# Kernel tuning notes

Hardware: AMD Instinct MI355X
Metric: run time of the kernel (lower is better)

The kernel has to match this reference:

```python
import jax, jax.numpy as jnp
import numpy as np

NEG_SLOPE = 0.2


def gat_conv(x, src, dst, W, att_src, att_dst, bias, heads, out_ch):
    # x: [N, Fin]; src/dst: [E] (self-loops already included)
    N = x.shape[0]
    h = (x @ W).reshape(N, heads, out_ch)                      # [N, H, C]
    a_s = jnp.einsum('nhc,hc->nh', h, att_src)                 # [N, H]
    a_d = jnp.einsum('nhc,hc->nh', h, att_dst)                 # [N, H]
    e = jax.nn.leaky_relu(a_s[src] + a_d[dst], NEG_SLOPE)      # [E, H]
    # segment softmax over incoming edges of each dst node
    e_max = jax.ops.segment_max(e, dst, num_segments=N)        # [N, H]
    p = jnp.exp(e - e_max[dst])                                # [E, H]
    denom = jax.ops.segment_sum(p, dst, num_segments=N)        # [N, H]
    alpha = p / denom[dst]                                     # [E, H]
    msg = h[src] * alpha[:, :, None]                           # [E, H, C]
    out = jax.ops.segment_sum(msg, dst, num_segments=N)        # [N, H, C]
    return out.reshape(N, heads * out_ch) + bias


def setup_inputs() -> dict:
    key = jax.random.key(0)
    ks = jax.random.split(key, 10)
    N, E, F_IN, HID, HEADS, NCLS = 100000, 3200000, 512, 8, 8, 16
    x = jax.random.normal(ks[0], (N, F_IN), dtype=jnp.float32)
    edge_index = jax.random.randint(ks[1], (2, E), 0, N, dtype=jnp.int64)
    s = 1.0 / np.sqrt(F_IN)
    W1 = jax.random.uniform(ks[2], (F_IN, HEADS * HID), jnp.float32, -s, s)
    att_src1 = jax.random.normal(ks[3], (HEADS, HID), jnp.float32) * 0.1
    att_dst1 = jax.random.normal(ks[4], (HEADS, HID), jnp.float32) * 0.1
    b1 = jnp.zeros((HEADS * HID,), jnp.float32)
    s2 = 1.0 / np.sqrt(HEADS * HID)
    W2 = jax.random.uniform(ks[5], (HEADS * HID, NCLS), jnp.float32, -s2, s2)
    att_src2 = jax.random.normal(ks[6], (1, NCLS), jnp.float32) * 0.1
    att_dst2 = jax.random.normal(ks[7], (1, NCLS), jnp.float32) * 0.1
    b2 = jnp.zeros((NCLS,), jnp.float32)
    return {"x": x, "edge_index": edge_index, "W1": W1, "att_src1": att_src1,
            "att_dst1": att_dst1, "b1": b1, "W2": W2, "att_src2": att_src2,
            "att_dst2": att_dst2, "b2": b2}


def reference(x, edge_index, W1, att_src1, att_dst1, b1, W2, att_src2, att_dst2, b2):
    N = x.shape[0]
    loops = jnp.arange(N, dtype=edge_index.dtype)
    src = jnp.concatenate([edge_index[0], loops])  # PyG add_self_loops=True
    dst = jnp.concatenate([edge_index[1], loops])
    # eval mode: F.dropout is identity
    h = gat_conv(x, src, dst, W1, att_src1, att_dst1, b1, heads=8, out_ch=8)
    h = jax.nn.elu(h)
    out = gat_conv(h, src, dst, W2, att_src2, att_dst2, b2, heads=1, out_ch=16)
    return out
```

## Files before the change

kernel.cpp:

```cpp
#include <hip/hip_runtime.h>

#define F_IN 512
#define F1 64
#define NCLS 16
#define NEG_SLOPE 0.2f

typedef __attribute__((ext_vector_type(8))) short short8;
typedef __attribute__((ext_vector_type(4))) float f32x4;

__device__ __forceinline__ unsigned short f2bf(float f) {
    unsigned u = __float_as_uint(f);
    return (unsigned short)((u + 0x7fffu + ((u >> 16) & 1u)) >> 16);
}
__device__ __forceinline__ float bf2f(unsigned short u) {
    return __uint_as_float(((unsigned)u) << 16);
}


__global__ __launch_bounds__(64) void k_detect(const int* __restrict__ ei, int E,
                                               unsigned* __restrict__ mode) {
    int t = threadIdx.x;
    unsigned nz = 0;
    int lim = (E > 256) ? 256 : E;
    for (int k = t; k < lim; k += 64) nz |= (unsigned)ei[2 * k + 1];
    for (int off = 1; off < 64; off <<= 1) nz |= __shfl_xor(nz, off);
    if (t == 0) *mode = (nz == 0) ? 1u : 0u;
}


__device__ __forceinline__ void gemm1_tile(const float* __restrict__ x,
                                           const float* __restrict__ W1,
                                           const float* __restrict__ att_s,
                                           const float* __restrict__ att_d,
                                           unsigned short* __restrict__ h1b,
                                           float* __restrict__ a_s1,
                                           float* __restrict__ a_d1,
                                           int N, int row0,
                                           unsigned short (*Abuf)[40],
                                           unsigned short (*BbufT)[40]) {
    const int tid = threadIdx.x;
    const int w = tid >> 6, lane = tid & 63;
    const int quad = lane >> 4, r16 = lane & 15;

    f32x4 acc[4];
#pragma unroll
    for (int t = 0; t < 4; t++) acc[t] = (f32x4){0.f, 0.f, 0.f, 0.f};

    const int a_row = tid >> 2;
    const int a_seg = (tid & 3) * 8;
    const int b_col = tid & 63;
    const int b_kq  = tid >> 6;
    const int ar = row0 + a_row;

    for (int k0 = 0; k0 < F_IN; k0 += 32) {
        {
            float4 v0 = make_float4(0.f, 0.f, 0.f, 0.f), v1 = v0;
            if (ar < N) {
                const float* xp = x + (size_t)ar * F_IN + k0 + a_seg;
                v0 = *(const float4*)xp;
                v1 = *(const float4*)(xp + 4);
            }
            short8 cv;
            cv[0] = (short)f2bf(v0.x); cv[1] = (short)f2bf(v0.y);
            cv[2] = (short)f2bf(v0.z); cv[3] = (short)f2bf(v0.w);
            cv[4] = (short)f2bf(v1.x); cv[5] = (short)f2bf(v1.y);
            cv[6] = (short)f2bf(v1.z); cv[7] = (short)f2bf(v1.w);
            *(short8*)&Abuf[a_row][a_seg] = cv;
        }
        {
            const float* wp = W1 + (size_t)(k0 + b_kq * 8) * F1 + b_col;
            short8 cv;
#pragma unroll
            for (int j = 0; j < 8; j++)
                cv[j] = (short)f2bf(wp[(size_t)j * F1]);
            *(short8*)&BbufT[b_col][b_kq * 8] = cv;
        }
        __syncthreads();

        short8 af = *(const short8*)&Abuf[w * 16 + r16][quad * 8];
#pragma unroll
        for (int t = 0; t < 4; t++) {
            short8 bf = *(const short8*)&BbufT[t * 16 + r16][quad * 8];
            acc[t] = __builtin_amdgcn_mfma_f32_16x16x32_bf16(af, bf, acc[t], 0, 0, 0);
        }
        __syncthreads();
    }

    float ats[4], atd[4];
#pragma unroll
    for (int t = 0; t < 4; t++) {
        ats[t] = att_s[t * 16 + r16];
        atd[t] = att_d[t * 16 + r16];
    }
#pragma unroll
    for (int r = 0; r < 4; r++) {
        int grow = row0 + w * 16 + quad * 4 + r;
        bool ok = grow < N;
        float ps[4], pd[4];
#pragma unroll
        for (int t = 0; t < 4; t++) {
            float vv = acc[t][r];
            if (ok) h1b[(size_t)grow * F1 + t * 16 + r16] = f2bf(vv);
            ps[t] = vv * ats[t];
            pd[t] = vv * atd[t];
        }
#pragma unroll
        for (int t = 0; t < 4; t++) {
            ps[t] += __shfl_xor(ps[t], 1); pd[t] += __shfl_xor(pd[t], 1);
            ps[t] += __shfl_xor(ps[t], 2); pd[t] += __shfl_xor(pd[t], 2);
            ps[t] += __shfl_xor(ps[t], 4); pd[t] += __shfl_xor(pd[t], 4);
        }
        if (ok && (r16 & 7) == 0) {
            int hh0 = r16 >> 3;
#pragma unroll
            for (int t = 0; t < 4; t++) {
                a_s1[(size_t)grow * 8 + t * 2 + hh0] = ps[t];
                a_d1[(size_t)grow * 8 + t * 2 + hh0] = pd[t];
            }
        }
    }
}


__global__ __launch_bounds__(256) void k_fusedA(const float* __restrict__ x,
                                                const float* __restrict__ W1,
                                                const float* __restrict__ att_s,
                                                const float* __restrict__ att_d,
                                                unsigned short* __restrict__ h1b,
                                                float* __restrict__ a_s1,
                                                float* __restrict__ a_d1, int N,
                                                const int* __restrict__ ei,
                                                const unsigned* __restrict__ mode,
                                                int* __restrict__ src32,
                                                int* __restrict__ dst32,
                                                unsigned* __restrict__ deg,
                                                unsigned* __restrict__ bucketCnt,
                                                int E, int ET, int nch,
                                                int nb, int shift) {
    __shared__ __align__(16) char smem[10240];
    unsigned b = blockIdx.x;
    if ((b & 1) == 0) {
        gemm1_tile(x, W1, att_s, att_d, h1b, a_s1, a_d1, N, (int)(b >> 1) * 64,
                   (unsigned short (*)[40])smem,
                   (unsigned short (*)[40])(smem + 5120));
        return;
    }
    unsigned* cntL = (unsigned*)smem;
    for (int i = threadIdx.x; i < 1024; i += 256) cntL[i] = 0u;
    __syncthreads();

    const unsigned stride = (unsigned)nch * 256u;
    unsigned t = (b >> 1) * 256u + threadIdx.x;
    bool m64 = (*mode != 0u);
    const long long* e64 = (const long long*)ei;
    unsigned i = t;
    for (; i + 3u * stride < (unsigned)ET; i += 4u * stride) {
        unsigned i0 = i, i1 = i + stride, i2 = i + 2u * stride, i3 = i + 3u * stride;
        int s0, v0, s1, v1, s2, v2, s3, v3;
        if (m64) {
            s0 = (int)e64[i0]; s1 = (int)e64[i1]; s2 = (int)e64[i2]; s3 = (int)e64[i3];
            v0 = (i0 < (unsigned)E) ? (int)e64[E + i0] : (int)(i0 - E);
            v1 = (i1 < (unsigned)E) ? (int)e64[E + i1] : (int)(i1 - E);
            v2 = (i2 < (unsigned)E) ? (int)e64[E + i2] : (int)(i2 - E);
            v3 = (i3 < (unsigned)E) ? (int)e64[E + i3] : (int)(i3 - E);
        } else {
            s0 = ei[i0]; s1 = ei[i1]; s2 = ei[i2]; s3 = ei[i3];
            v0 = (i0 < (unsigned)E) ? ei[E + i0] : (int)(i0 - E);
            v1 = (i1 < (unsigned)E) ? ei[E + i1] : (int)(i1 - E);
            v2 = (i2 < (unsigned)E) ? ei[E + i2] : (int)(i2 - E);
            v3 = (i3 < (unsigned)E) ? ei[E + i3] : (int)(i3 - E);
        }
        if (i0 >= (unsigned)E) s0 = (int)(i0 - E);
        if (i1 >= (unsigned)E) s1 = (int)(i1 - E);
        if (i2 >= (unsigned)E) s2 = (int)(i2 - E);
        if (i3 >= (unsigned)E) s3 = (int)(i3 - E);
        s0 = s0 < 0 ? 0 : (s0 >= N ? N - 1 : s0);  v0 = v0 < 0 ? 0 : (v0 >= N ? N - 1 : v0);
        s1 = s1 < 0 ? 0 : (s1 >= N ? N - 1 : s1);  v1 = v1 < 0 ? 0 : (v1 >= N ? N - 1 : v1);
        s2 = s2 < 0 ? 0 : (s2 >= N ? N - 1 : s2);  v2 = v2 < 0 ? 0 : (v2 >= N ? N - 1 : v2);
        s3 = s3 < 0 ? 0 : (s3 >= N ? N - 1 : s3);  v3 = v3 < 0 ? 0 : (v3 >= N ? N - 1 : v3);
        src32[i0] = s0; dst32[i0] = v0;
        src32[i1] = s1; dst32[i1] = v1;
        src32[i2] = s2; dst32[i2] = v2;
        src32[i3] = s3; dst32[i3] = v3;
        atomicAdd(&deg[v0], 1u);
        atomicAdd(&deg[v1], 1u);
        atomicAdd(&deg[v2], 1u);
        atomicAdd(&deg[v3], 1u);
        atomicAdd(&cntL[(unsigned)v0 >> shift], 1u);
        atomicAdd(&cntL[(unsigned)v1 >> shift], 1u);
        atomicAdd(&cntL[(unsigned)v2 >> shift], 1u);
        atomicAdd(&cntL[(unsigned)v3 >> shift], 1u);
    }
    for (; i < (unsigned)ET; i += stride) {
        int s, v;
        if (i < (unsigned)E) {
            if (m64) { s = (int)e64[i]; v = (int)e64[E + i]; }
            else     { s = ei[i];       v = ei[E + i]; }
        } else {
            s = v = (int)(i - E);
        }
        s = s < 0 ? 0 : (s >= N ? N - 1 : s);
        v = v < 0 ? 0 : (v >= N ? N - 1 : v);
        src32[i] = s; dst32[i] = v;
        atomicAdd(&deg[v], 1u);
        atomicAdd(&cntL[(unsigned)v >> shift], 1u);
    }
    __syncthreads();
    for (int k = threadIdx.x; k < nb; k += 256) {
        unsigned c = cntL[k];
        if (c) atomicAdd(&bucketCnt[k], c);
    }
}


__global__ __launch_bounds__(256) void k_fusedB(const float* __restrict__ x,
                                                const float* __restrict__ W1,
                                                const float* __restrict__ att_s,
                                                const float* __restrict__ att_d,
                                                unsigned short* __restrict__ h1b,
                                                float* __restrict__ a_s1,
                                                float* __restrict__ a_d1, int N,
                                                int rowSplit,
                                                const int* __restrict__ src32,
                                                const int* __restrict__ dst32,
                                                unsigned* __restrict__ bucketFill,
                                                unsigned* __restrict__ pairs,
                                                int ET, int nch,
                                                int nb, int shift) {
    __shared__ __align__(16) char smem[10240];
    unsigned b = blockIdx.x;
    if (b & 1) {
        gemm1_tile(x, W1, att_s, att_d, h1b, a_s1, a_d1, N,
                   rowSplit + (int)(b >> 1) * 64,
                   (unsigned short (*)[40])smem,
                   (unsigned short (*)[40])(smem + 5120));
        return;
    }
    unsigned* cntA = (unsigned*)smem;
    unsigned* ofsA = (unsigned*)(smem + 4096);
    unsigned* part = (unsigned*)(smem + 8192);
    const int t = threadIdx.x;
    const int chunk = (ET + nch - 1) / nch;
    const int cbase = (int)(b >> 1) * chunk;
    const int cend = (cbase + chunk < ET) ? cbase + chunk : ET;
    const unsigned lmask = (1u << shift) - 1u;

    for (int k = t; k < 1024; k += 256) cntA[k] = 0u;
    __syncthreads();
    for (int k = cbase + t; k < cend; k += 256)
        atomicAdd(&cntA[(unsigned)dst32[k] >> shift], 1u);
    __syncthreads();
    unsigned a0 = cntA[4 * t + 0], a1 = cntA[4 * t + 1];
    unsigned a2 = cntA[4 * t + 2], a3 = cntA[4 * t + 3];
    unsigned ssum = a0 + a1 + a2 + a3;
    part[t] = ssum;
    __syncthreads();
    for (int off = 1; off < 256; off <<= 1) {
        unsigned add = (t >= off) ? part[t - off] : 0u;
        __syncthreads();
        part[t] += add;
        __syncthreads();
    }
    unsigned excl = part[t] - ssum;
    ofsA[4 * t + 0] = excl;
    ofsA[4 * t + 1] = excl + a0;
    ofsA[4 * t + 2] = excl + a0 + a1;
    ofsA[4 * t + 3] = excl + a0 + a1 + a2;
    __syncthreads();
    for (int k = t; k < nb; k += 256) {
        unsigned c = cntA[k];
        unsigned g = c ? atomicAdd(&bucketFill[k], c) : 0u;
        cntA[k] = g - ofsA[k];
    }
    __syncthreads();
    for (int k = cbase + t; k < cend; k += 256) {
        int v = dst32[k];
        int s = src32[k];
        unsigned bb = (unsigned)v >> shift;
        unsigned slot = atomicAdd(&ofsA[bb], 1u);
        pairs[cntA[bb] + slot] = (unsigned)s | (((unsigned)v & lmask) << 20);
    }
}


__global__ __launch_bounds__(256) void k_tilesum(const unsigned* __restrict__ deg,
                                                 int N, unsigned* __restrict__ tileSum) {
    int tid = threadIdx.x;
    int v = blockIdx.x * 256 + tid;
    unsigned d = (v < N) ? deg[v] : 0u;
    for (int off = 1; off < 64; off <<= 1) d += __shfl_xor(d, off);
    __shared__ unsigned ps[4];
    int lane = tid & 63, wid = tid >> 6;
    if (lane == 0) ps[wid] = d;
    __syncthreads();
    if (tid == 0) tileSum[blockIdx.x] = ps[0] + ps[1] + ps[2] + ps[3];
}

__global__ __launch_bounds__(1024) void k_scan_tiles(const unsigned* __restrict__ tileSum,
                                                     int nt, unsigned* __restrict__ tileOfs) {
    __shared__ unsigned sbuf[1024];
    int t = threadIdx.x;
    unsigned val = (t < nt) ? tileSum[t] : 0u;
    sbuf[t] = val;
    __syncthreads();
    for (int off = 1; off < 1024; off <<= 1) {
        unsigned add = (t >= off) ? sbuf[t - off] : 0u;
        __syncthreads();
        sbuf[t] += add;
        __syncthreads();
    }
    if (t < nt) tileOfs[t] = sbuf[t] - val;
}

__global__ __launch_bounds__(1024) void k_scan_buckets(const unsigned* __restrict__ bucketCnt,
                                                       int nb,
                                                       unsigned* __restrict__ bucketOfs,
                                                       unsigned* __restrict__ bucketFill) {
    __shared__ unsigned sbuf[1024];
    int t = threadIdx.x;
    unsigned val = (t < nb) ? bucketCnt[t] : 0u;
    sbuf[t] = val;
    __syncthreads();
    for (int off = 1; off < 1024; off <<= 1) {
        unsigned add = (t >= off) ? sbuf[t - off] : 0u;
        __syncthreads();
        sbuf[t] += add;
        __syncthreads();
    }
    if (t < nb) {
        unsigned e = sbuf[t] - val;
        bucketOfs[t] = e;
        bucketFill[t] = e;
    }
}

__global__ __launch_bounds__(256) void k_rowptr(const unsigned* __restrict__ deg,
                                                const unsigned* __restrict__ tileOfs,
                                                unsigned* __restrict__ row_ptr,
                                                int N, int ET) {
    __shared__ unsigned sbuf[256];
    int t = threadIdx.x;
    int v = blockIdx.x * 256 + t;
    unsigned d = (v < N) ? deg[v] : 0u;
    sbuf[t] = d;
    __syncthreads();
    for (int off = 1; off < 256; off <<= 1) {
        unsigned add = (t >= off) ? sbuf[t - off] : 0u;
        __syncthreads();
        sbuf[t] += add;
        __syncthreads();
    }
    if (v < N) row_ptr[v] = tileOfs[blockIdx.x] + sbuf[t] - d;
    if (blockIdx.x == 0 && t == 0) row_ptr[N] = (unsigned)ET;
}


__global__ __launch_bounds__(256) void k_sort(const unsigned* __restrict__ pairs,
                                              const unsigned* __restrict__ bucketOfs,
                                              const unsigned* __restrict__ bucketCnt,
                                              const unsigned* __restrict__ row_ptr,
                                              unsigned* __restrict__ ssrc,
                                              int N, int shift) {
    __shared__ unsigned f[1024];
    __shared__ unsigned rbase[1024];
    const int b = blockIdx.x;
    const int t = threadIdx.x;
    const int nodes = 1 << shift;
    const int bbase = b << shift;
    for (int i = t; i < nodes; i += 256) {
        f[i] = 0u;
        int v = bbase + i;
        rbase[i] = (v < N) ? row_ptr[v] : 0u;
    }
    __syncthreads();
    const unsigned base = bucketOfs[b];
    const unsigned cnt = bucketCnt[b];
    for (unsigned i = (unsigned)t; i < cnt; i += 256u) {
        unsigned pk = pairs[base + i];
        unsigned s = pk & 0xFFFFFu;
        unsigned local = pk >> 20;
        unsigned pos = rbase[local] + atomicAdd(&f[local], 1u);
        ssrc[pos] = s;
    }
}


__global__ __launch_bounds__(256) void k_agg1(const unsigned short* __restrict__ h1b,
                                              const float* __restrict__ a_s1,
                                              const float* __restrict__ a_d1,
                                              const float* __restrict__ b1,
                                              const unsigned* __restrict__ row_ptr,
                                              const unsigned* __restrict__ ssrc,
                                              float* __restrict__ g, int N) {
    int wid = threadIdx.x >> 6, lane = threadIdx.x & 63;
    int v = blockIdx.x * 4 + wid;
    if (v >= N) return;
    unsigned base = row_ptr[v];
    unsigned deg = row_ptr[v + 1] - base;
    int h = lane >> 3;
    float adv = a_d1[(size_t)v * 8 + h];

    float denom = 0.f, acc = 0.f;
    unsigned j = 0;
    for (; j + 8 <= deg; j += 8) {
        unsigned s0 = ssrc[base + j + 0];
        unsigned s1 = ssrc[base + j + 1];
        unsigned s2 = ssrc[base + j + 2];
        unsigned s3 = ssrc[base + j + 3];
        unsigned s4 = ssrc[base + j + 4];
        unsigned s5 = ssrc[base + j + 5];
        unsigned s6 = ssrc[base + j + 6];
        unsigned s7 = ssrc[base + j + 7];
        float as0 = a_s1[(size_t)s0 * 8 + h];
        float as1 = a_s1[(size_t)s1 * 8 + h];
        float as2 = a_s1[(size_t)s2 * 8 + h];
        float as3 = a_s1[(size_t)s3 * 8 + h];
        float as4 = a_s1[(size_t)s4 * 8 + h];
        float as5 = a_s1[(size_t)s5 * 8 + h];
        float as6 = a_s1[(size_t)s6 * 8 + h];
        float as7 = a_s1[(size_t)s7 * 8 + h];
        float h0 = bf2f(h1b[(size_t)s0 * F1 + lane]);
        float h1 = bf2f(h1b[(size_t)s1 * F1 + lane]);
        float h2v = bf2f(h1b[(size_t)s2 * F1 + lane]);
        float h3 = bf2f(h1b[(size_t)s3 * F1 + lane]);
        float h4 = bf2f(h1b[(size_t)s4 * F1 + lane]);
        float h5 = bf2f(h1b[(size_t)s5 * F1 + lane]);
        float h6 = bf2f(h1b[(size_t)s6 * F1 + lane]);
        float h7 = bf2f(h1b[(size_t)s7 * F1 + lane]);
        float e0 = as0 + adv; e0 = e0 > 0.f ? e0 : NEG_SLOPE * e0; float p0 = __expf(e0);
        float e1 = as1 + adv; e1 = e1 > 0.f ? e1 : NEG_SLOPE * e1; float p1 = __expf(e1);
        float e2 = as2 + adv; e2 = e2 > 0.f ? e2 : NEG_SLOPE * e2; float p2 = __expf(e2);
        float e3 = as3 + adv; e3 = e3 > 0.f ? e3 : NEG_SLOPE * e3; float p3 = __expf(e3);
        float e4 = as4 + adv; e4 = e4 > 0.f ? e4 : NEG_SLOPE * e4; float p4 = __expf(e4);
        float e5 = as5 + adv; e5 = e5 > 0.f ? e5 : NEG_SLOPE * e5; float p5 = __expf(e5);
        float e6 = as6 + adv; e6 = e6 > 0.f ? e6 : NEG_SLOPE * e6; float p6 = __expf(e6);
        float e7 = as7 + adv; e7 = e7 > 0.f ? e7 : NEG_SLOPE * e7; float p7 = __expf(e7);
        denom += ((p0 + p1) + (p2 + p3)) + ((p4 + p5) + (p6 + p7));
        acc = fmaf(h0, p0, acc);
        acc = fmaf(h1, p1, acc);
        acc = fmaf(h2v, p2, acc);
        acc = fmaf(h3, p3, acc);
        acc = fmaf(h4, p4, acc);
        acc = fmaf(h5, p5, acc);
        acc = fmaf(h6, p6, acc);
        acc = fmaf(h7, p7, acc);
    }
    for (; j < deg; j++) {
        unsigned s = ssrc[base + j];
        float as = a_s1[(size_t)s * 8 + h];
        float hv = bf2f(h1b[(size_t)s * F1 + lane]);
        float e = as + adv; e = e > 0.f ? e : NEG_SLOPE * e;
        float p = __expf(e);
        denom += p;
        acc = fmaf(hv, p, acc);
    }
    float t = acc * (1.0f / denom) + b1[lane];
    g[(size_t)v * F1 + lane] = t > 0.f ? t : (__expf(t) - 1.f);
}


__global__ __launch_bounds__(256) void k_gemm2(const float* __restrict__ g,
                                               const float* __restrict__ W2,
                                               const float* __restrict__ as2w,
                                               const float* __restrict__ ad2w,
                                               float* __restrict__ h2,
                                               float* __restrict__ a_s2,
                                               float* __restrict__ a_d2, int N) {
    __shared__ float W2s[F1][NCLS];
    int tid = threadIdx.x;
    for (int i = tid; i < F1 * NCLS; i += 256) ((float*)W2s)[i] = W2[i];
    __syncthreads();
    int lane = tid & 63, wid = tid >> 6;
    int n = blockIdx.x * 16 + wid * 4 + (lane >> 4);
    int c = lane & 15;
    if (n >= N) return;
    float acc = 0.f;
#pragma unroll
    for (int k4 = 0; k4 < 16; k4++) {
        float4 gv = *(const float4*)(g + (size_t)n * F1 + k4 * 4);
        acc = fmaf(gv.x, W2s[k4 * 4 + 0][c], acc);
        acc = fmaf(gv.y, W2s[k4 * 4 + 1][c], acc);
        acc = fmaf(gv.z, W2s[k4 * 4 + 2][c], acc);
        acc = fmaf(gv.w, W2s[k4 * 4 + 3][c], acc);
    }
    h2[(size_t)n * NCLS + c] = acc;
    float s = acc * as2w[c];
    float d = acc * ad2w[c];
    s += __shfl_xor(s, 1); s += __shfl_xor(s, 2); s += __shfl_xor(s, 4); s += __shfl_xor(s, 8);
    d += __shfl_xor(d, 1); d += __shfl_xor(d, 2); d += __shfl_xor(d, 4); d += __shfl_xor(d, 8);
    if (c == 0) { a_s2[n] = s; a_d2[n] = d; }
}


__global__ __launch_bounds__(256) void k_agg2(const float* __restrict__ h2,
                                              const float* __restrict__ a_s2,
                                              const float* __restrict__ a_d2,
                                              const float* __restrict__ b2,
                                              const unsigned* __restrict__ row_ptr,
                                              const unsigned* __restrict__ ssrc,
                                              float* __restrict__ out, int N) {
    int wid = threadIdx.x >> 6, lane = threadIdx.x & 63;
    int v = blockIdx.x * 4 + wid;
    if (v >= N) return;
    unsigned base = row_ptr[v];
    unsigned deg = row_ptr[v + 1] - base;
    float adv = a_d2[v];
    int sub = lane >> 4, c = lane & 15;

    float denom = 0.f, acc = 0.f;
    unsigned j = sub;
    for (; j + 12 < deg; j += 16) {
        unsigned s0 = ssrc[base + j + 0];
        unsigned s1 = ssrc[base + j + 4];
        unsigned s2 = ssrc[base + j + 8];
        unsigned s3 = ssrc[base + j + 12];
        float as0 = a_s2[s0];
        float as1 = a_s2[s1];
        float as2 = a_s2[s2];
        float as3 = a_s2[s3];
        float h0 = h2[(size_t)s0 * NCLS + c];
        float h1v = h2[(size_t)s1 * NCLS + c];
        float h2v = h2[(size_t)s2 * NCLS + c];
        float h3 = h2[(size_t)s3 * NCLS + c];
        float e0 = as0 + adv; e0 = e0 > 0.f ? e0 : NEG_SLOPE * e0; float p0 = __expf(e0);
        float e1 = as1 + adv; e1 = e1 > 0.f ? e1 : NEG_SLOPE * e1; float p1 = __expf(e1);
        float e2 = as2 + adv; e2 = e2 > 0.f ? e2 : NEG_SLOPE * e2; float p2 = __expf(e2);
        float e3 = as3 + adv; e3 = e3 > 0.f ? e3 : NEG_SLOPE * e3; float p3 = __expf(e3);
        denom += (p0 + p1) + (p2 + p3);
        acc = fmaf(h0, p0, acc);
        acc = fmaf(h1v, p1, acc);
        acc = fmaf(h2v, p2, acc);
        acc = fmaf(h3, p3, acc);
    }
    for (; j < deg; j += 4) {
        unsigned s = ssrc[base + j];
        float as = a_s2[s];
        float hv = h2[(size_t)s * NCLS + c];
        float e = as + adv; e = e > 0.f ? e : NEG_SLOPE * e;
        float p = __expf(e);
        denom += p;
        acc = fmaf(hv, p, acc);
    }
    acc += __shfl_xor(acc, 16);
    acc += __shfl_xor(acc, 32);
    denom += __shfl_xor(denom, 16);
    denom += __shfl_xor(denom, 32);
    if (lane < 16) {
        out[(size_t)v * NCLS + c] = acc * (1.0f / denom) + b2[c];
    }
}


static inline size_t algn(size_t x) { return (x + 255) & ~(size_t)255; }

extern "C" void kernel_launch(void* const* d_in, const int* in_sizes, int n_in,
                              void* d_out, int out_size, void* d_ws, size_t ws_size,
                              hipStream_t stream) {
    const float* x   = (const float*)d_in[0];
    const int* ei    = (const int*)d_in[1];
    const float* W1  = (const float*)d_in[2];
    const float* as1 = (const float*)d_in[3];
    const float* ad1 = (const float*)d_in[4];
    const float* b1  = (const float*)d_in[5];
    const float* W2  = (const float*)d_in[6];
    const float* as2 = (const float*)d_in[7];
    const float* ad2 = (const float*)d_in[8];
    const float* b2  = (const float*)d_in[9];

    const int N = in_sizes[0] / F_IN;
    const int E = in_sizes[1] / 2;
    const int ET = E + N;
    const int nt = (N + 255) / 256;

    int shift = 8;
    int nb = (N + 255) >> 8;
    while (nb > 1024) { shift++; nb = (N + (1 << shift) - 1) >> shift; }

    const int GA_T = ((N / 2) + 63) / 64;
    const int rowSplit = GA_T * 64;
    const int GB_T = (N - rowSplit + 63) / 64;

    char* p = (char*)d_ws;
    unsigned short* h1b = (unsigned short*)p;  p += algn((size_t)N * F1 * 2);
    float* g    = (float*)p;      p += algn((size_t)N * F1 * 4);
    float* a_s1 = (float*)p;      p += algn((size_t)N * 8 * 4);
    float* a_d1 = (float*)p;      p += algn((size_t)N * 8 * 4);
    float* h2   = (float*)p;      p += algn((size_t)N * NCLS * 4);
    float* a_s2 = (float*)p;      p += algn((size_t)N * 4);
    float* a_d2 = (float*)p;      p += algn((size_t)N * 4);
    unsigned* deg     = (unsigned*)p;  p += algn((size_t)N * 4);
    unsigned* row_ptr = (unsigned*)p;  p += algn((size_t)(N + 1) * 4);
    unsigned* tileSum = (unsigned*)p;  p += algn((size_t)1024 * 4);
    unsigned* tileOfs = (unsigned*)p;  p += algn((size_t)1024 * 4);
    unsigned* bucketCnt  = (unsigned*)p;  p += algn((size_t)1024 * 4);
    unsigned* bucketOfs  = (unsigned*)p;  p += algn((size_t)1024 * 4);
    unsigned* bucketFill = (unsigned*)p;  p += algn((size_t)1024 * 4);
    unsigned* mode    = (unsigned*)p;  p += algn(256);
    int* src32 = (int*)p;              p += algn((size_t)ET * 4);
    int* dst32 = (int*)p;              p += algn((size_t)ET * 4);
    unsigned* ssrc = (unsigned*)p;     p += algn((size_t)ET * 4);
    unsigned* pairs = (unsigned*)g;

    hipMemsetAsync(deg, 0, (size_t)N * 4, stream);
    hipMemsetAsync(bucketCnt, 0, (size_t)nb * 4, stream);

    dim3 b256(256);
    k_detect<<<dim3(1), dim3(64), 0, stream>>>(ei, E, mode);

    k_fusedA<<<dim3(2 * GA_T), b256, 0, stream>>>(x, W1, as1, ad1, h1b, a_s1, a_d1, N,
                                                  ei, mode, src32, dst32, deg, bucketCnt,
                                                  E, ET, GA_T, nb, shift);

    k_tilesum<<<dim3(nt), b256, 0, stream>>>(deg, N, tileSum);
    k_scan_tiles<<<dim3(1), dim3(1024), 0, stream>>>(tileSum, nt, tileOfs);
    k_rowptr<<<dim3(nt), b256, 0, stream>>>(deg, tileOfs, row_ptr, N, ET);
    k_scan_buckets<<<dim3(1), dim3(1024), 0, stream>>>(bucketCnt, nb, bucketOfs, bucketFill);

    k_fusedB<<<dim3(2 * GB_T), b256, 0, stream>>>(x, W1, as1, ad1, h1b, a_s1, a_d1, N,
                                                  rowSplit, src32, dst32, bucketFill,
                                                  pairs, ET, GB_T, nb, shift);

    k_sort<<<dim3(nb), b256, 0, stream>>>(pairs, bucketOfs, bucketCnt, row_ptr, ssrc, N, shift);

    k_agg1<<<dim3((N + 3) / 4), b256, 0, stream>>>(h1b, a_s1, a_d1, b1, row_ptr, ssrc, g, N);
    k_gemm2<<<dim3((N + 15) / 16), b256, 0, stream>>>(g, W2, as2, ad2, h2, a_s2, a_d2, N);
    k_agg2<<<dim3((N + 3) / 4), b256, 0, stream>>>(h2, a_s2, a_d2, b2, row_ptr, ssrc,
                                                   (float*)d_out, N);
}
```

Measured before the change: 687.8 us.

## Derive CSR row pointers inside bucket sort, drop per-node degree pass

Removes the global per-node degree atomics, the src32/dst32 intermediate arrays and the three degree-scan kernels. The bucket sort now builds a local histogram and scan of destination nodes per bucket and writes row_ptr itself. Edge indices are decoded straight from the input edge list in both fused kernels, which cuts global atomics and intermediate memory traffic. In exchange the raw (possibly int64) edge list is read twice more, and each sort block does an extra pass over its pairs plus a shared-memory scan.

```diff
diff --git a/kernel.cpp b/kernel.cpp
--- a/kernel.cpp
+++ b/kernel.cpp
@@ -25,6 +25,30 @@
     for (int k = t; k < lim; k += 64) nz |= (unsigned)ei[2 * k + 1];
     for (int off = 1; off < 64; off <<= 1) nz |= __shfl_xor(nz, off);
     if (t == 0) *mode = (nz == 0) ? 1u : 0u;
+}
+
+__device__ __forceinline__ void decode_edge(const int* __restrict__ ei,
+                                            const long long* __restrict__ e64,
+                                            bool m64, unsigned i, int E, int N,
+                                            int& s, int& v) {
+    if (i < (unsigned)E) {
+        if (m64) { s = (int)e64[i]; v = (int)e64[E + i]; }
+        else     { s = ei[i];       v = ei[E + i]; }
+    } else {
+        s = (int)(i - (unsigned)E);
+        v = s;
+    }
+    s = s < 0 ? 0 : (s >= N ? N - 1 : s);
+    v = v < 0 ? 0 : (v >= N ? N - 1 : v);
+}
+
+__device__ __forceinline__ int decode_dst(const int* __restrict__ ei,
+                                          const long long* __restrict__ e64,
+                                          bool m64, unsigned i, int E, int N) {
+    int v;
+    if (i < (unsigned)E) v = m64 ? (int)e64[E + i] : ei[E + i];
+    else                 v = (int)(i - (unsigned)E);
+    return v < 0 ? 0 : (v >= N ? N - 1 : v);
 }
 
 
@@ -131,9 +155,6 @@
                                                 float* __restrict__ a_d1, int N,
                                                 const int* __restrict__ ei,
                                                 const unsigned* __restrict__ mode,
-                                                int* __restrict__ src32,
-                                                int* __restrict__ dst32,
-                                                unsigned* __restrict__ deg,
                                                 unsigned* __restrict__ bucketCnt,
                                                 int E, int ET, int nch,
                                                 int nb, int shift) {
@@ -150,59 +171,21 @@
     __syncthreads();
 
     const unsigned stride = (unsigned)nch * 256u;
-    unsigned t = (b >> 1) * 256u + threadIdx.x;
     bool m64 = (*mode != 0u);
     const long long* e64 = (const long long*)ei;
-    unsigned i = t;
+    unsigned i = (b >> 1) * 256u + threadIdx.x;
     for (; i + 3u * stride < (unsigned)ET; i += 4u * stride) {
-        unsigned i0 = i, i1 = i + stride, i2 = i + 2u * stride, i3 = i + 3u * stride;
-        int s0, v0, s1, v1, s2, v2, s3, v3;
-        if (m64) {
-            s0 = (int)e64[i0]; s1 = (int)e64[i1]; s2 = (int)e64[i2]; s3 = (int)e64[i3];
-            v0 = (i0 < (unsigned)E) ? (int)e64[E + i0] : (int)(i0 - E);
-            v1 = (i1 < (unsigned)E) ? (int)e64[E + i1] : (int)(i1 - E);
-            v2 = (i2 < (unsigned)E) ? (int)e64[E + i2] : (int)(i2 - E);
-            v3 = (i3 < (unsigned)E) ? (int)e64[E + i3] : (int)(i3 - E);
-        } else {
-            s0 = ei[i0]; s1 = ei[i1]; s2 = ei[i2]; s3 = ei[i3];
-            v0 = (i0 < (unsigned)E) ? ei[E + i0] : (int)(i0 - E);
-            v1 = (i1 < (unsigned)E) ? ei[E + i1] : (int)(i1 - E);
-            v2 = (i2 < (unsigned)E) ? ei[E + i2] : (int)(i2 - E);
-            v3 = (i3 < (unsigned)E) ? ei[E + i3] : (int)(i3 - E);
-        }
-        if (i0 >= (unsigned)E) s0 = (int)(i0 - E);
-        if (i1 >= (unsigned)E) s1 = (int)(i1 - E);
-        if (i2 >= (unsigned)E) s2 = (int)(i2 - E);
-        if (i3 >= (unsigned)E) s3 = (int)(i3 - E);
-        s0 = s0 < 0 ? 0 : (s0 >= N ? N - 1 : s0);  v0 = v0 < 0 ? 0 : (v0 >= N ? N - 1 : v0);
-        s1 = s1 < 0 ? 0 : (s1 >= N ? N - 1 : s1);  v1 = v1 < 0 ? 0 : (v1 >= N ? N - 1 : v1);
-        s2 = s2 < 0 ? 0 : (s2 >= N ? N - 1 : s2);  v2 = v2 < 0 ? 0 : (v2 >= N ? N - 1 : v2);
-        s3 = s3 < 0 ? 0 : (s3 >= N ? N - 1 : s3);  v3 = v3 < 0 ? 0 : (v3 >= N ? N - 1 : v3);
-        src32[i0] = s0; dst32[i0] = v0;
-        src32[i1] = s1; dst32[i1] = v1;
-        src32[i2] = s2; dst32[i2] = v2;
-        src32[i3] = s3; dst32[i3] = v3;
-        atomicAdd(&deg[v0], 1u);
-        atomicAdd(&deg[v1], 1u);
-        atomicAdd(&deg[v2], 1u);
-        atomicAdd(&deg[v3], 1u);
+        int v0 = decode_dst(ei, e64, m64, i, E, N);
+        int v1 = decode_dst(ei, e64, m64, i + stride, E, N);
+        int v2 = decode_dst(ei, e64, m64, i + 2u * stride, E, N);
+        int v3 = decode_dst(ei, e64, m64, i + 3u * stride, E, N);
         atomicAdd(&cntL[(unsigned)v0 >> shift], 1u);
         atomicAdd(&cntL[(unsigned)v1 >> shift], 1u);
         atomicAdd(&cntL[(unsigned)v2 >> shift], 1u);
         atomicAdd(&cntL[(unsigned)v3 >> shift], 1u);
     }
     for (; i < (unsigned)ET; i += stride) {
-        int s, v;
-        if (i < (unsigned)E) {
-            if (m64) { s = (int)e64[i]; v = (int)e64[E + i]; }
-            else     { s = ei[i];       v = ei[E + i]; }
-        } else {
-            s = v = (int)(i - E);
-        }
-        s = s < 0 ? 0 : (s >= N ? N - 1 : s);
-        v = v < 0 ? 0 : (v >= N ? N - 1 : v);
-        src32[i] = s; dst32[i] = v;
-        atomicAdd(&deg[v], 1u);
+        int v = decode_dst(ei, e64, m64, i, E, N);
         atomicAdd(&cntL[(unsigned)v >> shift], 1u);
     }
     __syncthreads();
@@ -221,11 +204,11 @@
                                                 float* __restrict__ a_s1,
                                                 float* __restrict__ a_d1, int N,
                                                 int rowSplit,
-                                                const int* __restrict__ src32,
-                                                const int* __restrict__ dst32,
+                                                const int* __restrict__ ei,
+                                                const unsigned* __restrict__ mode,
                                                 unsigned* __restrict__ bucketFill,
                                                 unsigned* __restrict__ pairs,
-                                                int ET, int nch,
+                                                int E, int ET, int nch,
                                                 int nb, int shift) {
     __shared__ __align__(16) char smem[10240];
     unsigned b = blockIdx.x;
@@ -244,11 +227,15 @@
     const int cbase = (int)(b >> 1) * chunk;
     const int cend = (cbase + chunk < ET) ? cbase + chunk : ET;
     const unsigned lmask = (1u << shift) - 1u;
+    bool m64 = (*mode != 0u);
+    const long long* e64 = (const long long*)ei;
 
     for (int k = t; k < 1024; k += 256) cntA[k] = 0u;
     __syncthreads();
-    for (int k = cbase + t; k < cend; k += 256)
-        atomicAdd(&cntA[(unsigned)dst32[k] >> shift], 1u);
+    for (int k = cbase + t; k < cend; k += 256) {
+        int v = decode_dst(ei, e64, m64, (unsigned)k, E, N);
+        atomicAdd(&cntA[(unsigned)v >> shift], 1u);
+    }
     __syncthreads();
     unsigned a0 = cntA[4 * t + 0], a1 = cntA[4 * t + 1];
     unsigned a2 = cntA[4 * t + 2], a3 = cntA[4 * t + 3];
@@ -274,8 +261,8 @@
     }
     __syncthreads();
     for (int k = cbase + t; k < cend; k += 256) {
-        int v = dst32[k];
-        int s = src32[k];
+        int s, v;
+        decode_edge(ei, e64, m64, (unsigned)k, E, N, s, v);
         unsigned bb = (unsigned)v >> shift;
         unsigned slot = atomicAdd(&ofsA[bb], 1u);
         pairs[cntA[bb] + slot] = (unsigned)s | (((unsigned)v & lmask) << 20);
@@ -283,39 +270,12 @@
 }
 
 
-__global__ __launch_bounds__(256) void k_tilesum(const unsigned* __restrict__ deg,
-                                                 int N, unsigned* __restrict__ tileSum) {
-    int tid = threadIdx.x;
-    int v = blockIdx.x * 256 + tid;
-    unsigned d = (v < N) ? deg[v] : 0u;
-    for (int off = 1; off < 64; off <<= 1) d += __shfl_xor(d, off);
-    __shared__ unsigned ps[4];
-    int lane = tid & 63, wid = tid >> 6;
-    if (lane == 0) ps[wid] = d;
-    __syncthreads();
-    if (tid == 0) tileSum[blockIdx.x] = ps[0] + ps[1] + ps[2] + ps[3];
-}
-
-__global__ __launch_bounds__(1024) void k_scan_tiles(const unsigned* __restrict__ tileSum,
-                                                     int nt, unsigned* __restrict__ tileOfs) {
-    __shared__ unsigned sbuf[1024];
-    int t = threadIdx.x;
-    unsigned val = (t < nt) ? tileSum[t] : 0u;
-    sbuf[t] = val;
-    __syncthreads();
-    for (int off = 1; off < 1024; off <<= 1) {
-        unsigned add = (t >= off) ? sbuf[t - off] : 0u;
-        __syncthreads();
-        sbuf[t] += add;
-        __syncthreads();
-    }
-    if (t < nt) tileOfs[t] = sbuf[t] - val;
-}
-
 __global__ __launch_bounds__(1024) void k_scan_buckets(const unsigned* __restrict__ bucketCnt,
-                                                       int nb,
+                                                       int nb, int ET,
                                                        unsigned* __restrict__ bucketOfs,
-                                                       unsigned* __restrict__ bucketFill) {
+                                                       unsigned* __restrict__ bucketFill,
+                                                       unsigned* __restrict__ row_ptr,
+                                                       int N) {
     __shared__ unsigned sbuf[1024];
     int t = threadIdx.x;
     unsigned val = (t < nb) ? bucketCnt[t] : 0u;
@@ -332,55 +292,62 @@
         bucketOfs[t] = e;
         bucketFill[t] = e;
     }
-}
-
-__global__ __launch_bounds__(256) void k_rowptr(const unsigned* __restrict__ deg,
-                                                const unsigned* __restrict__ tileOfs,
-                                                unsigned* __restrict__ row_ptr,
-                                                int N, int ET) {
-    __shared__ unsigned sbuf[256];
-    int t = threadIdx.x;
-    int v = blockIdx.x * 256 + t;
-    unsigned d = (v < N) ? deg[v] : 0u;
-    sbuf[t] = d;
-    __syncthreads();
-    for (int off = 1; off < 256; off <<= 1) {
-        unsigned add = (t >= off) ? sbuf[t - off] : 0u;
-        __syncthreads();
-        sbuf[t] += add;
-        __syncthreads();
-    }
-    if (v < N) row_ptr[v] = tileOfs[blockIdx.x] + sbuf[t] - d;
-    if (blockIdx.x == 0 && t == 0) row_ptr[N] = (unsigned)ET;
+    if (t == 0) row_ptr[N] = (unsigned)ET;
 }
 
 
 __global__ __launch_bounds__(256) void k_sort(const unsigned* __restrict__ pairs,
                                               const unsigned* __restrict__ bucketOfs,
                                               const unsigned* __restrict__ bucketCnt,
-                                              const unsigned* __restrict__ row_ptr,
+                                              unsigned* __restrict__ row_ptr,
                                               unsigned* __restrict__ ssrc,
                                               int N, int shift) {
     __shared__ unsigned f[1024];
-    __shared__ unsigned rbase[1024];
+    __shared__ unsigned part[256];
     const int b = blockIdx.x;
     const int t = threadIdx.x;
     const int nodes = 1 << shift;
     const int bbase = b << shift;
-    for (int i = t; i < nodes; i += 256) {
-        f[i] = 0u;
-        int v = bbase + i;
-        rbase[i] = (v < N) ? row_ptr[v] : 0u;
-    }
+    for (int i = t; i < 1024; i += 256) f[i] = 0u;
     __syncthreads();
     const unsigned base = bucketOfs[b];
     const unsigned cnt = bucketCnt[b];
+    for (unsigned i = (unsigned)t; i < cnt; i += 256u)
+        atomicAdd(&f[pairs[base + i] >> 20], 1u);
+    __syncthreads();
+    unsigned a0 = f[4 * t + 0], a1 = f[4 * t + 1];
+    unsigned a2 = f[4 * t + 2], a3 = f[4 * t + 3];
+    unsigned ssum = a0 + a1 + a2 + a3;
+    part[t] = ssum;
+    __syncthreads();
+    for (int off = 1; off < 256; off <<= 1) {
+        unsigned add = (t >= off) ? part[t - off] : 0u;
+        __syncthreads();
+        part[t] += add;
+        __syncthreads();
+    }
+    unsigned excl = part[t] - ssum;
+    unsigned c0 = base + excl;
+    unsigned c1 = c0 + a0;
+    unsigned c2 = c1 + a1;
+    unsigned c3 = c2 + a2;
+    {
+        int v0 = bbase + 4 * t;
+        if (v0 + 0 < N && 4 * t + 0 < nodes) row_ptr[v0 + 0] = c0;
+        if (v0 + 1 < N && 4 * t + 1 < nodes) row_ptr[v0 + 1] = c1;
+        if (v0 + 2 < N && 4 * t + 2 < nodes) row_ptr[v0 + 2] = c2;
+        if (v0 + 3 < N && 4 * t + 3 < nodes) row_ptr[v0 + 3] = c3;
+    }
+    f[4 * t + 0] = c0;
+    f[4 * t + 1] = c1;
+    f[4 * t + 2] = c2;
+    f[4 * t + 3] = c3;
+    __syncthreads();
     for (unsigned i = (unsigned)t; i < cnt; i += 256u) {
         unsigned pk = pairs[base + i];
-        unsigned s = pk & 0xFFFFFu;
         unsigned local = pk >> 20;
-        unsigned pos = rbase[local] + atomicAdd(&f[local], 1u);
-        ssrc[pos] = s;
+        unsigned pos = atomicAdd(&f[local], 1u);
+        ssrc[pos] = pk & 0xFFFFFu;
     }
 }
 
@@ -570,7 +537,6 @@
     const int N = in_sizes[0] / F_IN;
     const int E = in_sizes[1] / 2;
     const int ET = E + N;
-    const int nt = (N + 255) / 256;
 
     int shift = 8;
     int nb = (N + 255) >> 8;
@@ -588,37 +554,29 @@
     float* h2   = (float*)p;      p += algn((size_t)N * NCLS * 4);
     float* a_s2 = (float*)p;      p += algn((size_t)N * 4);
     float* a_d2 = (float*)p;      p += algn((size_t)N * 4);
-    unsigned* deg     = (unsigned*)p;  p += algn((size_t)N * 4);
     unsigned* row_ptr = (unsigned*)p;  p += algn((size_t)(N + 1) * 4);
-    unsigned* tileSum = (unsigned*)p;  p += algn((size_t)1024 * 4);
-    unsigned* tileOfs = (unsigned*)p;  p += algn((size_t)1024 * 4);
     unsigned* bucketCnt  = (unsigned*)p;  p += algn((size_t)1024 * 4);
     unsigned* bucketOfs  = (unsigned*)p;  p += algn((size_t)1024 * 4);
     unsigned* bucketFill = (unsigned*)p;  p += algn((size_t)1024 * 4);
     unsigned* mode    = (unsigned*)p;  p += algn(256);
-    int* src32 = (int*)p;              p += algn((size_t)ET * 4);
-    int* dst32 = (int*)p;              p += algn((size_t)ET * 4);
     unsigned* ssrc = (unsigned*)p;     p += algn((size_t)ET * 4);
     unsigned* pairs = (unsigned*)g;
 
-    hipMemsetAsync(deg, 0, (size_t)N * 4, stream);
     hipMemsetAsync(bucketCnt, 0, (size_t)nb * 4, stream);
 
     dim3 b256(256);
     k_detect<<<dim3(1), dim3(64), 0, stream>>>(ei, E, mode);
 
     k_fusedA<<<dim3(2 * GA_T), b256, 0, stream>>>(x, W1, as1, ad1, h1b, a_s1, a_d1, N,
-                                                  ei, mode, src32, dst32, deg, bucketCnt,
+                                                  ei, mode, bucketCnt,
                                                   E, ET, GA_T, nb, shift);
 
-    k_tilesum<<<dim3(nt), b256, 0, stream>>>(deg, N, tileSum);
-    k_scan_tiles<<<dim3(1), dim3(1024), 0, stream>>>(tileSum, nt, tileOfs);
-    k_rowptr<<<dim3(nt), b256, 0, stream>>>(deg, tileOfs, row_ptr, N, ET);
-    k_scan_buckets<<<dim3(1), dim3(1024), 0, stream>>>(bucketCnt, nb, bucketOfs, bucketFill);
+    k_scan_buckets<<<dim3(1), dim3(1024), 0, stream>>>(bucketCnt, nb, ET, bucketOfs,
+                                                       bucketFill, row_ptr, N);
 
     k_fusedB<<<dim3(2 * GB_T), b256, 0, stream>>>(x, W1, as1, ad1, h1b, a_s1, a_d1, N,
-                                                  rowSplit, src32, dst32, bucketFill,
-                                                  pairs, ET, GB_T, nb, shift);
+                                                  rowSplit, ei, mode, bucketFill,
+                                                  pairs, E, ET, GB_T, nb, shift);
 
     k_sort<<<dim3(nb), b256, 0, stream>>>(pairs, bucketOfs, bucketCnt, row_ptr, ssrc, N, shift);
 
```

Measured after the change: 640.2 us. 6.9% less time.
